# Kernel optimization log

Hardware: AMD Instinct MI355X
Metric: run time of the kernel (lower is better)

Reference implementation:

```python
import jax, jax.numpy as jnp
import numpy as np

N_NODES = 50000
N_EDGES = 800000
D_IN, D_HID, D_OUT = 128, 256, 128


def _glorot(key, shape):
    fan_in, fan_out = shape[1], shape[0]
    lim = (6.0 / (fan_in + fan_out)) ** 0.5
    return jax.random.uniform(key, shape, jnp.float32, -lim, lim)


def setup_inputs() -> dict:
    key = jax.random.key(0)
    ks = jax.random.split(key, 8)
    x = jax.random.normal(ks[0], (N_NODES, D_IN), dtype=jnp.float32)
    edge_index = jax.random.randint(ks[1], (2, N_EDGES), 0, N_NODES, dtype=jnp.int64)
    # Layer 1: SAGEConv(D_IN -> D_HID); Layer 2: SAGEConv(D_HID -> D_OUT)
    # PyG SAGEConv: out = lin_l(mean_aggr(x_j)) + lin_r(x); bias lives in lin_l.
    Wl1 = _glorot(ks[2], (D_HID, D_IN))
    bl1 = jnp.zeros((D_HID,), jnp.float32)
    Wr1 = _glorot(ks[3], (D_HID, D_IN))
    Wl2 = _glorot(ks[4], (D_OUT, D_HID))
    bl2 = jnp.zeros((D_OUT,), jnp.float32)
    Wr2 = _glorot(ks[5], (D_OUT, D_HID))
    return {"x": x, "Wl1": Wl1, "bl1": bl1, "Wr1": Wr1,
            "Wl2": Wl2, "bl2": bl2, "Wr2": Wr2, "edge_index": edge_index}


def _sage_conv(x, src, dst, deg_inv, Wl, bl, Wr):
    # gather source features per edge, sum into dst buckets, normalize by in-degree
    msg_sum = jax.ops.segment_sum(x[src], dst, num_segments=N_NODES)  # [N, d_in]
    mean = msg_sum * deg_inv  # mean aggregation; isolated nodes -> zeros
    return mean @ Wl.T + bl + x @ Wr.T


def reference(x, Wl1, bl1, Wr1, Wl2, bl2, Wr2, edge_index):
    src, dst = edge_index[0], edge_index[1]
    deg = jax.ops.segment_sum(jnp.ones((N_EDGES,), jnp.float32), dst,
                              num_segments=N_NODES)
    deg_inv = (1.0 / jnp.maximum(deg, 1.0))[:, None]  # [N, 1]
    h = _sage_conv(x, src, dst, deg_inv, Wl1, bl1, Wr1)
    h = jax.nn.relu(h)  # dropout is identity in eval mode
    out = _sage_conv(h, src, dst, deg_inv, Wl2, bl2, Wr2)
    return out
```

## Files before the change

### kernel.cpp

```cpp
#include <hip/hip_runtime.h>
#include <hip/hip_fp16.h>

#define N_NODES 50000
#define N_EDGES 800000
#define D_IN 128
#define D_HID 256
#define D_OUT 128
#define NCHUNK 196
#define GEMM_GRID 512

typedef _Float16 f16x8 __attribute__((ext_vector_type(8)));
typedef float f32x4 __attribute__((ext_vector_type(4)));


__global__ __launch_bounds__(256)
void prep_kernel(const float* __restrict__ x, __half2* __restrict__ xb,
                 const float* __restrict__ Wl1, const float* __restrict__ Wr1,
                 const float* __restrict__ Wl2, const float* __restrict__ Wr2,
                 __half2* __restrict__ wl1h, __half2* __restrict__ wr1h,
                 __half2* __restrict__ wl2h, __half2* __restrict__ wr2h,
                 int* __restrict__ deg) {
    int b = blockIdx.x;
    if (b < 12500) {
        int i = b * 256 + threadIdx.x;
        xb[i] = __float22half2_rn(((const float2*)x)[i]);
    } else if (b < 12564) {
        int i = (b - 12500) * 256 + threadIdx.x;
        wl1h[i] = __float22half2_rn(((const float2*)Wl1)[i]);
        wr1h[i] = __float22half2_rn(((const float2*)Wr1)[i]);
        wl2h[i] = __float22half2_rn(((const float2*)Wl2)[i]);
        wr2h[i] = __float22half2_rn(((const float2*)Wr2)[i]);
    } else {
        int i = (b - 12564) * 256 + threadIdx.x;
        if (i < N_NODES) deg[i] = 0;
    }
}


__global__ void deg_rank_kernel(const int* __restrict__ dst, int* __restrict__ deg,
                                int* __restrict__ rank) {
    int i = blockIdx.x * blockDim.x + threadIdx.x;
    if (i < N_EDGES) rank[i] = atomicAdd(&deg[dst[i]], 1);
}

__global__ void chunk_sum(const int* __restrict__ deg, int* __restrict__ partial) {
    __shared__ int s[256];
    int i = blockIdx.x * 256 + threadIdx.x;
    s[threadIdx.x] = (i < N_NODES) ? deg[i] : 0;
    __syncthreads();
    for (int off = 128; off > 0; off >>= 1) {
        if (threadIdx.x < off) s[threadIdx.x] += s[threadIdx.x + off];
        __syncthreads();
    }
    if (threadIdx.x == 0) partial[blockIdx.x] = s[0];
}

__global__ void chunk_scan(const int* __restrict__ partial, int* __restrict__ chunkOff) {
    __shared__ int s[256];
    int tid = threadIdx.x;
    int v = (tid < NCHUNK) ? partial[tid] : 0;
    s[tid] = v;
    __syncthreads();
    for (int off = 1; off < 256; off <<= 1) {
        int t = (tid >= off) ? s[tid - off] : 0;
        __syncthreads();
        s[tid] += t;
        __syncthreads();
    }
    if (tid < NCHUNK) chunkOff[tid] = s[tid] - v;
}

__global__ void scatter_scan(const int* __restrict__ deg, const int* __restrict__ chunkOff,
                             int* __restrict__ row_ptr, float* __restrict__ deg_inv) {
    __shared__ int s[256];
    int tid = threadIdx.x;
    int i = blockIdx.x * 256 + tid;
    int v = (i < N_NODES) ? deg[i] : 0;
    s[tid] = v;
    __syncthreads();
    for (int off = 1; off < 256; off <<= 1) {
        int t = (tid >= off) ? s[tid - off] : 0;
        __syncthreads();
        s[tid] += t;
        __syncthreads();
    }
    if (i < N_NODES) {
        int rp = chunkOff[blockIdx.x] + s[tid] - v;
        row_ptr[i] = rp;
        deg_inv[i] = 1.0f / fmaxf((float)v, 1.0f);
        if (i == N_NODES - 1) row_ptr[N_NODES] = N_EDGES;
    }
}

__global__ void fill_csr(const int* __restrict__ src, const int* __restrict__ dst,
                         const int* __restrict__ rank, const int* __restrict__ row_ptr,
                         int* __restrict__ csr_src) {
    int e = blockIdx.x * blockDim.x + threadIdx.x;
    if (e < N_EDGES) {
        csr_src[row_ptr[dst[e]] + rank[e]] = src[e];
    }
}


__device__ __forceinline__ float4 load_row4(const float4* __restrict__ feat4,
                                            int src, int s) {
    return feat4[(size_t)src * 16 + s];
}

__device__ __forceinline__ void add_row(const float4& v, float (&acc)[8]) {
    const __half2* hp = (const __half2*)&v;
    float2 f0 = __half22float2(hp[0]);
    float2 f1 = __half22float2(hp[1]);
    float2 f2 = __half22float2(hp[2]);
    float2 f3 = __half22float2(hp[3]);
    acc[0] += f0.x; acc[1] += f0.y;
    acc[2] += f1.x; acc[3] += f1.y;
    acc[4] += f2.x; acc[5] += f2.y;
    acc[6] += f3.x; acc[7] += f3.y;
}

template<bool ACCUM_F32>
__device__ __forceinline__ void gather_core(const __half2* __restrict__ feat,
                                            const int* __restrict__ row_ptr,
                                            const int* __restrict__ csr_src,
                                            const float* __restrict__ deg_inv,
                                            __half2* __restrict__ outh,
                                            float* __restrict__ outf) {
    const float4* feat4 = (const float4*)feat;
    const int lane = threadIdx.x & 63;
    const int g = lane >> 4;
    const int s = lane & 15;
    const int n = blockIdx.x * 4 + (threadIdx.x >> 6);
    const int beg = row_ptr[n];
    const int end = row_ptr[n + 1];
    float acc[8] = {};
    int e = beg;
    for (; e + 16 <= end; e += 16) {
        int s0 = csr_src[e + g];
        int s1 = csr_src[e + 4 + g];
        int s2 = csr_src[e + 8 + g];
        int s3 = csr_src[e + 12 + g];
        float4 v0 = load_row4(feat4, s0, s);
        float4 v1 = load_row4(feat4, s1, s);
        float4 v2 = load_row4(feat4, s2, s);
        float4 v3 = load_row4(feat4, s3, s);
        add_row(v0, acc);
        add_row(v1, acc);
        add_row(v2, acc);
        add_row(v3, acc);
    }
    for (; e + 4 <= end; e += 4) {
        int s0 = csr_src[e + g];
        float4 v0 = load_row4(feat4, s0, s);
        add_row(v0, acc);
    }
    if (e < end) {
        if (g < end - e) {
            int s0 = csr_src[e + g];
            float4 v0 = load_row4(feat4, s0, s);
            add_row(v0, acc);
        }
    }
    #pragma unroll
    for (int j = 0; j < 8; ++j) {
        acc[j] += __shfl_xor(acc[j], 16);
        acc[j] += __shfl_xor(acc[j], 32);
    }
    if (g == 0) {
        float di = deg_inv[n];
        if (ACCUM_F32) {
            float4* orow = (float4*)(outf + (size_t)n * 128);
            float4 o0 = orow[s * 2];
            float4 o1 = orow[s * 2 + 1];
            o0.x += acc[0] * di; o0.y += acc[1] * di;
            o0.z += acc[2] * di; o0.w += acc[3] * di;
            o1.x += acc[4] * di; o1.y += acc[5] * di;
            o1.z += acc[6] * di; o1.w += acc[7] * di;
            orow[s * 2] = o0;
            orow[s * 2 + 1] = o1;
        } else {
            float4 o;
            __half2* op = (__half2*)&o;
            op[0] = __float22half2_rn(make_float2(acc[0] * di, acc[1] * di));
            op[1] = __float22half2_rn(make_float2(acc[2] * di, acc[3] * di));
            op[2] = __float22half2_rn(make_float2(acc[4] * di, acc[5] * di));
            op[3] = __float22half2_rn(make_float2(acc[6] * di, acc[7] * di));
            ((float4*)(outh + (size_t)n * 64))[s] = o;
        }
    }
}

__global__ __launch_bounds__(256)
void gather_mean_h(const __half2* __restrict__ feat, const int* __restrict__ row_ptr,
                   const int* __restrict__ csr_src, const float* __restrict__ deg_inv,
                   __half2* __restrict__ outv) {
    gather_core<false>(feat, row_ptr, csr_src, deg_inv, outv, nullptr);
}

__global__ __launch_bounds__(256)
void gather_mean_add_f32(const __half2* __restrict__ feat, const int* __restrict__ row_ptr,
                         const int* __restrict__ csr_src, const float* __restrict__ deg_inv,
                         float* __restrict__ out) {
    gather_core<true>(feat, row_ptr, csr_src, deg_inv, nullptr, out);
}


__global__ __launch_bounds__(256, 2)
void gemm_l1(const __half* __restrict__ Aa, const __half* __restrict__ Ba,
             const __half* __restrict__ Ab, const __half* __restrict__ Bb,
             const float* __restrict__ bias, __half* __restrict__ H) {
    const int lane = threadIdx.x & 63;
    const int wave = threadIdx.x >> 6;
    const int quad = lane >> 4;
    const int l16 = lane & 15;
    const int koff = quad * 8;

    f16x8 bf[2][4][4];
    #pragma unroll
    for (int p = 0; p < 2; ++p) {
        const __half* __restrict__ B = p ? Bb : Ba;
        #pragma unroll
        for (int kc = 0; kc < 4; ++kc)
            #pragma unroll
            for (int nt = 0; nt < 4; ++nt)
                bf[p][kc][nt] = *(const f16x8*)(
                    B + (size_t)(wave * 64 + nt * 16 + l16) * D_IN + kc * 32 + koff);
    }
    float bv[4];
    #pragma unroll
    for (int nt = 0; nt < 4; ++nt) bv[nt] = bias[wave * 64 + nt * 16 + l16];

    const int NT = N_NODES / 16;
    const int g = gridDim.x;

    auto loadA = [&](int t, f16x8 (&a)[2][4]) {
        const size_t arow = (size_t)(t * 16 + l16) * D_IN + koff;
        #pragma unroll
        for (int kc = 0; kc < 4; ++kc) {
            a[0][kc] = *(const f16x8*)(Aa + arow + kc * 32);
            a[1][kc] = *(const f16x8*)(Ab + arow + kc * 32);
        }
    };
    auto step = [&](int tile, const f16x8 (&a)[2][4]) {
        f32x4 acc[4] = {};
        #pragma unroll
        for (int p = 0; p < 2; ++p)
            #pragma unroll
            for (int kc = 0; kc < 4; ++kc)
                #pragma unroll
                for (int nt = 0; nt < 4; ++nt)
                    acc[nt] = __builtin_amdgcn_mfma_f32_16x16x32_f16(
                        a[p][kc], bf[p][kc][nt], acc[nt], 0, 0, 0);
        #pragma unroll
        for (int nt = 0; nt < 4; ++nt) {
            int col = wave * 64 + nt * 16 + l16;
            #pragma unroll
            for (int r = 0; r < 4; ++r) {
                int row = tile * 16 + quad * 4 + r;
                H[(size_t)row * D_HID + col] =
                    __float2half(fmaxf(acc[nt][r] + bv[nt], 0.f));
            }
        }
    };

    f16x8 A0[2][4], A1[2][4];
    int tile = blockIdx.x;
    loadA(tile, A0);
    while (true) {
        if (tile + g < NT) loadA(tile + g, A1);
        step(tile, A0);
        tile += g;
        if (tile >= NT) break;
        if (tile + g < NT) loadA(tile + g, A0);
        step(tile, A1);
        tile += g;
        if (tile >= NT) break;
    }
}

__global__ __launch_bounds__(256, 2)
void gemm_l2(const __half* __restrict__ Hh, const __half* __restrict__ B0,
             const __half* __restrict__ B1, const float* __restrict__ bias,
             __half* __restrict__ P, float* __restrict__ out) {
    const int lane = threadIdx.x & 63;
    const int wave = threadIdx.x >> 6;
    const int quad = lane >> 4;
    const int l16 = lane & 15;
    const int koff = quad * 8;

    f16x8 bf0[8][2], bf1[8][2];
    #pragma unroll
    for (int kc = 0; kc < 8; ++kc)
        #pragma unroll
        for (int nt = 0; nt < 2; ++nt) {
            size_t brow = (size_t)(wave * 32 + nt * 16 + l16) * D_HID + kc * 32 + koff;
            bf0[kc][nt] = *(const f16x8*)(B0 + brow);
            bf1[kc][nt] = *(const f16x8*)(B1 + brow);
        }
    float bv[2];
    #pragma unroll
    for (int nt = 0; nt < 2; ++nt) bv[nt] = bias[wave * 32 + nt * 16 + l16];

    const int NT = N_NODES / 16;
    const int g = gridDim.x;

    auto loadA = [&](int t, f16x8 (&a)[8]) {
        const size_t arow = (size_t)(t * 16 + l16) * D_HID + koff;
        #pragma unroll
        for (int kc = 0; kc < 8; ++kc)
            a[kc] = *(const f16x8*)(Hh + arow + kc * 32);
    };
    auto step = [&](int tile, const f16x8 (&a)[8]) {
        f32x4 acc0[2] = {};
        f32x4 acc1[2] = {};
        #pragma unroll
        for (int kc = 0; kc < 8; ++kc)
            #pragma unroll
            for (int nt = 0; nt < 2; ++nt) {
                acc0[nt] = __builtin_amdgcn_mfma_f32_16x16x32_f16(
                    a[kc], bf0[kc][nt], acc0[nt], 0, 0, 0);
                acc1[nt] = __builtin_amdgcn_mfma_f32_16x16x32_f16(
                    a[kc], bf1[kc][nt], acc1[nt], 0, 0, 0);
            }
        #pragma unroll
        for (int nt = 0; nt < 2; ++nt) {
            int col = wave * 32 + nt * 16 + l16;
            #pragma unroll
            for (int r = 0; r < 4; ++r) {
                int row = tile * 16 + quad * 4 + r;
                P[(size_t)row * D_OUT + col] = __float2half(acc0[nt][r]);
                out[(size_t)row * D_OUT + col] = acc1[nt][r] + bv[nt];
            }
        }
    };

    f16x8 A0[8], A1[8];
    int tile = blockIdx.x;
    loadA(tile, A0);
    while (true) {
        if (tile + g < NT) loadA(tile + g, A1);
        step(tile, A0);
        tile += g;
        if (tile >= NT) break;
        if (tile + g < NT) loadA(tile + g, A0);
        step(tile, A1);
        tile += g;
        if (tile >= NT) break;
    }
}

extern "C" void kernel_launch(void* const* d_in, const int* in_sizes, int n_in,
                              void* d_out, int out_size, void* d_ws, size_t ws_size,
                              hipStream_t stream) {
    const float* x   = (const float*)d_in[0];
    const float* Wl1 = (const float*)d_in[1];
    const float* bl1 = (const float*)d_in[2];
    const float* Wr1 = (const float*)d_in[3];
    const float* Wl2 = (const float*)d_in[4];
    const float* bl2 = (const float*)d_in[5];
    const float* Wr2 = (const float*)d_in[6];
    const int*   ei  = (const int*)d_in[7];
    const int* src = ei;
    const int* dst = ei + N_EDGES;
    float* out = (float*)d_out;

    char* w = (char*)d_ws;
    auto alloc = [&](size_t bytes) {
        char* r = w;
        w += (bytes + 255) & ~(size_t)255;
        return r;
    };
    int*     deg       = (int*)alloc((size_t)N_NODES * 4);
    int*     row_ptr   = (int*)alloc((size_t)(N_NODES + 1) * 4);
    int*     rank      = (int*)alloc((size_t)N_EDGES * 4);
    int*     partial   = (int*)alloc(NCHUNK * 4);
    int*     chunkOff  = (int*)alloc(NCHUNK * 4);
    int*     csr_src   = (int*)alloc((size_t)N_EDGES * 4);
    float*   deg_inv   = (float*)alloc((size_t)N_NODES * 4);
    __half2* xb        = (__half2*)alloc((size_t)N_NODES * 64 * 4);
    __half2* mean1     = (__half2*)alloc((size_t)N_NODES * 64 * 4);
    __half*  h         = (__half*)alloc((size_t)N_NODES * 256 * 2);
    __half2* pb        = (__half2*)alloc((size_t)N_NODES * 64 * 4);
    __half*  wl1h      = (__half*)alloc(4 * 32768 * 2);
    __half*  wr1h = wl1h + 32768;
    __half*  wl2h = wr1h + 32768;
    __half*  wr2h = wl2h + 32768;

    prep_kernel<<<12760, 256, 0, stream>>>(x, xb, Wl1, Wr1, Wl2, Wr2,
        (__half2*)wl1h, (__half2*)wr1h, (__half2*)wl2h, (__half2*)wr2h, deg);

    deg_rank_kernel<<<(N_EDGES + 255) / 256, 256, 0, stream>>>(dst, deg, rank);
    chunk_sum<<<NCHUNK, 256, 0, stream>>>(deg, partial);
    chunk_scan<<<1, 256, 0, stream>>>(partial, chunkOff);
    scatter_scan<<<NCHUNK, 256, 0, stream>>>(deg, chunkOff, row_ptr, deg_inv);
    fill_csr<<<(N_EDGES + 255) / 256, 256, 0, stream>>>(src, dst, rank, row_ptr, csr_src);

    gather_mean_h<<<12500, 256, 0, stream>>>(xb, row_ptr, csr_src, deg_inv, mean1);
    gemm_l1<<<GEMM_GRID, 256, 0, stream>>>(
        (const __half*)mean1, wl1h, (const __half*)xb, wr1h, bl1, h);

    gemm_l2<<<GEMM_GRID, 256, 0, stream>>>(
        h, wl2h, wr2h, bl2, (__half*)pb, out);
    gather_mean_add_f32<<<12500, 256, 0, stream>>>(pb, row_ptr, csr_src, deg_inv, out);
}
```

Measured before the change: 258.6 us.

## Fuse layer-1 and layer-2 GEMMs through LDS and fold chunk scan into scatter

Merges the two GEMM kernels into one, so each 16-row hidden tile stays in double-buffered shared memory and feeds the layer-2 MFMAs directly. This removes the 25.6 MB fp16 hidden-activation write and read and one launch. It also drops the single-block chunk_scan kernel by having each scatter_scan block reduce its own prefix from the partial sums. The price is more register pressure from holding both layers' weights (launch bounds drop to 1 block per CU), plus a block barrier per tile.

```diff
diff --git a/kernel.cpp b/kernel.cpp
--- a/kernel.cpp
+++ b/kernel.cpp
@@ -55,26 +55,21 @@
     if (threadIdx.x == 0) partial[blockIdx.x] = s[0];
 }
 
-__global__ void chunk_scan(const int* __restrict__ partial, int* __restrict__ chunkOff) {
-    __shared__ int s[256];
-    int tid = threadIdx.x;
-    int v = (tid < NCHUNK) ? partial[tid] : 0;
-    s[tid] = v;
-    __syncthreads();
-    for (int off = 1; off < 256; off <<= 1) {
-        int t = (tid >= off) ? s[tid - off] : 0;
-        __syncthreads();
-        s[tid] += t;
-        __syncthreads();
-    }
-    if (tid < NCHUNK) chunkOff[tid] = s[tid] - v;
-}
-
-__global__ void scatter_scan(const int* __restrict__ deg, const int* __restrict__ chunkOff,
+__global__ void scatter_scan(const int* __restrict__ deg, const int* __restrict__ partial,
                              int* __restrict__ row_ptr, float* __restrict__ deg_inv) {
     __shared__ int s[256];
-    int tid = threadIdx.x;
-    int i = blockIdx.x * 256 + tid;
+    __shared__ int base_s;
+    const int tid = threadIdx.x;
+    const int bid = blockIdx.x;
+    s[tid] = (tid < bid) ? partial[tid] : 0;
+    __syncthreads();
+    for (int off = 128; off > 0; off >>= 1) {
+        if (tid < off) s[tid] += s[tid + off];
+        __syncthreads();
+    }
+    if (tid == 0) base_s = s[0];
+    __syncthreads();
+    int i = bid * 256 + tid;
     int v = (i < N_NODES) ? deg[i] : 0;
     s[tid] = v;
     __syncthreads();
@@ -85,7 +80,7 @@
         __syncthreads();
     }
     if (i < N_NODES) {
-        int rp = chunkOff[blockIdx.x] + s[tid] - v;
+        int rp = base_s + s[tid] - v;
         row_ptr[i] = rp;
         deg_inv[i] = 1.0f / fmaxf((float)v, 1.0f);
         if (i == N_NODES - 1) row_ptr[N_NODES] = N_EDGES;
@@ -205,17 +200,23 @@
 }
 
 
-__global__ __launch_bounds__(256, 2)
-void gemm_l1(const __half* __restrict__ Aa, const __half* __restrict__ Ba,
-             const __half* __restrict__ Ab, const __half* __restrict__ Bb,
-             const float* __restrict__ bias, __half* __restrict__ H) {
+#define HPAD 264
+
+__global__ __launch_bounds__(256, 1)
+void gemm_fused(const __half* __restrict__ Aa, const __half* __restrict__ Ba,
+                const __half* __restrict__ Ab, const __half* __restrict__ Bb,
+                const float* __restrict__ bias1,
+                const __half* __restrict__ B20, const __half* __restrict__ B21,
+                const float* __restrict__ bias2,
+                __half* __restrict__ P, float* __restrict__ out) {
+    __shared__ __half hlds[2][16][HPAD];
     const int lane = threadIdx.x & 63;
     const int wave = threadIdx.x >> 6;
     const int quad = lane >> 4;
     const int l16 = lane & 15;
     const int koff = quad * 8;
 
-    f16x8 bf[2][4][4];
+    f16x8 bf1[2][4][4];
     #pragma unroll
     for (int p = 0; p < 2; ++p) {
         const __half* __restrict__ B = p ? Bb : Ba;
@@ -223,12 +224,25 @@
         for (int kc = 0; kc < 4; ++kc)
             #pragma unroll
             for (int nt = 0; nt < 4; ++nt)
-                bf[p][kc][nt] = *(const f16x8*)(
+                bf1[p][kc][nt] = *(const f16x8*)(
                     B + (size_t)(wave * 64 + nt * 16 + l16) * D_IN + kc * 32 + koff);
     }
-    float bv[4];
-    #pragma unroll
-    for (int nt = 0; nt < 4; ++nt) bv[nt] = bias[wave * 64 + nt * 16 + l16];
+    float bv1[4];
+    #pragma unroll
+    for (int nt = 0; nt < 4; ++nt) bv1[nt] = bias1[wave * 64 + nt * 16 + l16];
+
+    f16x8 bf20[8][2], bf21[8][2];
+    #pragma unroll
+    for (int kc = 0; kc < 8; ++kc)
+        #pragma unroll
+        for (int nt = 0; nt < 2; ++nt) {
+            size_t brow = (size_t)(wave * 32 + nt * 16 + l16) * D_HID + kc * 32 + koff;
+            bf20[kc][nt] = *(const f16x8*)(B20 + brow);
+            bf21[kc][nt] = *(const f16x8*)(B21 + brow);
+        }
+    float bv2[2];
+    #pragma unroll
+    for (int nt = 0; nt < 2; ++nt) bv2[nt] = bias2[wave * 32 + nt * 16 + l16];
 
     const int NT = N_NODES / 16;
     const int g = gridDim.x;
@@ -241,109 +255,64 @@
             a[1][kc] = *(const f16x8*)(Ab + arow + kc * 32);
         }
     };
-    auto step = [&](int tile, const f16x8 (&a)[2][4]) {
-        f32x4 acc[4] = {};
+
+    auto step = [&](int tile, const f16x8 (&a)[2][4], int buf) {
+        f32x4 acc1[4] = {};
         #pragma unroll
         for (int p = 0; p < 2; ++p)
             #pragma unroll
             for (int kc = 0; kc < 4; ++kc)
                 #pragma unroll
                 for (int nt = 0; nt < 4; ++nt)
-                    acc[nt] = __builtin_amdgcn_mfma_f32_16x16x32_f16(
-                        a[p][kc], bf[p][kc][nt], acc[nt], 0, 0, 0);
+                    acc1[nt] = __builtin_amdgcn_mfma_f32_16x16x32_f16(
+                        a[p][kc], bf1[p][kc][nt], acc1[nt], 0, 0, 0);
         #pragma unroll
         for (int nt = 0; nt < 4; ++nt) {
             int col = wave * 64 + nt * 16 + l16;
             #pragma unroll
+            for (int r = 0; r < 4; ++r)
+                hlds[buf][quad * 4 + r][col] =
+                    __float2half(fmaxf(acc1[nt][r] + bv1[nt], 0.f));
+        }
+        __syncthreads();
+        f32x4 acc20[2] = {};
+        f32x4 acc21[2] = {};
+        #pragma unroll
+        for (int kc = 0; kc < 8; ++kc) {
+            f16x8 a2 = *(const f16x8*)&hlds[buf][l16][kc * 32 + koff];
+            #pragma unroll
+            for (int nt = 0; nt < 2; ++nt) {
+                acc20[nt] = __builtin_amdgcn_mfma_f32_16x16x32_f16(
+                    a2, bf20[kc][nt], acc20[nt], 0, 0, 0);
+                acc21[nt] = __builtin_amdgcn_mfma_f32_16x16x32_f16(
+                    a2, bf21[kc][nt], acc21[nt], 0, 0, 0);
+            }
+        }
+        #pragma unroll
+        for (int nt = 0; nt < 2; ++nt) {
+            int col = wave * 32 + nt * 16 + l16;
+            #pragma unroll
             for (int r = 0; r < 4; ++r) {
                 int row = tile * 16 + quad * 4 + r;
-                H[(size_t)row * D_HID + col] =
-                    __float2half(fmaxf(acc[nt][r] + bv[nt], 0.f));
+                P[(size_t)row * D_OUT + col] = __float2half(acc20[nt][r]);
+                out[(size_t)row * D_OUT + col] = acc21[nt][r] + bv2[nt];
             }
         }
     };
 
     f16x8 A0[2][4], A1[2][4];
     int tile = blockIdx.x;
+    int buf = 0;
     loadA(tile, A0);
     while (true) {
         if (tile + g < NT) loadA(tile + g, A1);
-        step(tile, A0);
+        step(tile, A0, buf);
+        buf ^= 1;
         tile += g;
         if (tile >= NT) break;
         if (tile + g < NT) loadA(tile + g, A0);
-        step(tile, A1);
-        tile += g;
-        if (tile >= NT) break;
-    }
-}
-
-__global__ __launch_bounds__(256, 2)
-void gemm_l2(const __half* __restrict__ Hh, const __half* __restrict__ B0,
-             const __half* __restrict__ B1, const float* __restrict__ bias,
-             __half* __restrict__ P, float* __restrict__ out) {
-    const int lane = threadIdx.x & 63;
-    const int wave = threadIdx.x >> 6;
-    const int quad = lane >> 4;
-    const int l16 = lane & 15;
-    const int koff = quad * 8;
-
-    f16x8 bf0[8][2], bf1[8][2];
-    #pragma unroll
-    for (int kc = 0; kc < 8; ++kc)
-        #pragma unroll
-        for (int nt = 0; nt < 2; ++nt) {
-            size_t brow = (size_t)(wave * 32 + nt * 16 + l16) * D_HID + kc * 32 + koff;
-            bf0[kc][nt] = *(const f16x8*)(B0 + brow);
-            bf1[kc][nt] = *(const f16x8*)(B1 + brow);
-        }
-    float bv[2];
-    #pragma unroll
-    for (int nt = 0; nt < 2; ++nt) bv[nt] = bias[wave * 32 + nt * 16 + l16];
-
-    const int NT = N_NODES / 16;
-    const int g = gridDim.x;
-
-    auto loadA = [&](int t, f16x8 (&a)[8]) {
-        const size_t arow = (size_t)(t * 16 + l16) * D_HID + koff;
-        #pragma unroll
-        for (int kc = 0; kc < 8; ++kc)
-            a[kc] = *(const f16x8*)(Hh + arow + kc * 32);
-    };
-    auto step = [&](int tile, const f16x8 (&a)[8]) {
-        f32x4 acc0[2] = {};
-        f32x4 acc1[2] = {};
-        #pragma unroll
-        for (int kc = 0; kc < 8; ++kc)
-            #pragma unroll
-            for (int nt = 0; nt < 2; ++nt) {
-                acc0[nt] = __builtin_amdgcn_mfma_f32_16x16x32_f16(
-                    a[kc], bf0[kc][nt], acc0[nt], 0, 0, 0);
-                acc1[nt] = __builtin_amdgcn_mfma_f32_16x16x32_f16(
-                    a[kc], bf1[kc][nt], acc1[nt], 0, 0, 0);
-            }
-        #pragma unroll
-        for (int nt = 0; nt < 2; ++nt) {
-            int col = wave * 32 + nt * 16 + l16;
-            #pragma unroll
-            for (int r = 0; r < 4; ++r) {
-                int row = tile * 16 + quad * 4 + r;
-                P[(size_t)row * D_OUT + col] = __float2half(acc0[nt][r]);
-                out[(size_t)row * D_OUT + col] = acc1[nt][r] + bv[nt];
-            }
-        }
-    };
-
-    f16x8 A0[8], A1[8];
-    int tile = blockIdx.x;
-    loadA(tile, A0);
-    while (true) {
-        if (tile + g < NT) loadA(tile + g, A1);
-        step(tile, A0);
-        tile += g;
-        if (tile >= NT) break;
-        if (tile + g < NT) loadA(tile + g, A0);
-        step(tile, A1);
+        step(tile, A1, buf);
+        buf ^= 1;
         tile += g;
         if (tile >= NT) break;
     }
@@ -374,12 +343,10 @@
     int*     row_ptr   = (int*)alloc((size_t)(N_NODES + 1) * 4);
     int*     rank      = (int*)alloc((size_t)N_EDGES * 4);
     int*     partial   = (int*)alloc(NCHUNK * 4);
-    int*     chunkOff  = (int*)alloc(NCHUNK * 4);
     int*     csr_src   = (int*)alloc((size_t)N_EDGES * 4);
     float*   deg_inv   = (float*)alloc((size_t)N_NODES * 4);
     __half2* xb        = (__half2*)alloc((size_t)N_NODES * 64 * 4);
     __half2* mean1     = (__half2*)alloc((size_t)N_NODES * 64 * 4);
-    __half*  h         = (__half*)alloc((size_t)N_NODES * 256 * 2);
     __half2* pb        = (__half2*)alloc((size_t)N_NODES * 64 * 4);
     __half*  wl1h      = (__half*)alloc(4 * 32768 * 2);
     __half*  wr1h = wl1h + 32768;
@@ -391,15 +358,14 @@
 
     deg_rank_kernel<<<(N_EDGES + 255) / 256, 256, 0, stream>>>(dst, deg, rank);
     chunk_sum<<<NCHUNK, 256, 0, stream>>>(deg, partial);
-    chunk_scan<<<1, 256, 0, stream>>>(partial, chunkOff);
-    scatter_scan<<<NCHUNK, 256, 0, stream>>>(deg, chunkOff, row_ptr, deg_inv);
+    scatter_scan<<<NCHUNK, 256, 0, stream>>>(deg, partial, row_ptr, deg_inv);
     fill_csr<<<(N_EDGES + 255) / 256, 256, 0, stream>>>(src, dst, rank, row_ptr, csr_src);
 
     gather_mean_h<<<12500, 256, 0, stream>>>(xb, row_ptr, csr_src, deg_inv, mean1);
-    gemm_l1<<<GEMM_GRID, 256, 0, stream>>>(
-        (const __half*)mean1, wl1h, (const __half*)xb, wr1h, bl1, h);
-
-    gemm_l2<<<GEMM_GRID, 256, 0, stream>>>(
-        h, wl2h, wr2h, bl2, (__half*)pb, out);
+
+    gemm_fused<<<GEMM_GRID, 256, 0, stream>>>(
+        (const __half*)mean1, wl1h, (const __half*)xb, wr1h, bl1,
+        wl2h, wr2h, bl2, (__half*)pb, out);
+
     gather_mean_add_f32<<<12500, 256, 0, stream>>>(pb, row_ptr, csr_src, deg_inv, out);
 }
```

Measured after the change: 245.1 us. -5.2%, faster.
